# Optimization experiments

Hardware: AMD Instinct MI355X
Metric: run time of the kernel (lower is better)

Reference implementation:

```python
import math
import jax, jax.numpy as jnp
import numpy as np

DIM = 4096
N_HEADS = 32
N_KV_HEADS = 8
HEAD_DIM = DIM // N_HEADS        # 128
N_REP = N_HEADS // N_KV_HEADS    # 4
BSZ = 1
SEQ = 2048
ROPE_THETA = 500000.0


def setup_inputs() -> dict:
    key = jax.random.key(0)
    ks = jax.random.split(key, 5)
    scale = 1.0 / math.sqrt(DIM)
    x = jax.random.normal(ks[0], (BSZ, SEQ, DIM), dtype=jnp.float32)
    wq = jax.random.normal(ks[1], (N_HEADS * HEAD_DIM, DIM), dtype=jnp.float32) * scale
    wk = jax.random.normal(ks[2], (N_KV_HEADS * HEAD_DIM, DIM), dtype=jnp.float32) * scale
    wv = jax.random.normal(ks[3], (N_KV_HEADS * HEAD_DIM, DIM), dtype=jnp.float32) * scale
    wo = jax.random.normal(ks[4], (N_HEADS * HEAD_DIM, DIM), dtype=jnp.float32).T * scale
    wo = jnp.asarray(wo)  # [DIM, N_HEADS*HEAD_DIM] like nn.Linear(in=heads*hd, out=dim).weight
    # RoPE tables: freqs_cis[t, j] = exp(i * t * theta^{-2j/head_dim}), j in [0, head_dim/2)
    inv_freq = 1.0 / (ROPE_THETA ** (np.arange(0, HEAD_DIM, 2, dtype=np.float32) / HEAD_DIM))
    t = np.arange(SEQ, dtype=np.float32)
    ang = np.outer(t, inv_freq)  # [SEQ, HEAD_DIM//2]
    freqs_cos = jnp.asarray(np.cos(ang), dtype=jnp.float32)
    freqs_sin = jnp.asarray(np.sin(ang), dtype=jnp.float32)
    # additive causal mask [SEQ, SEQ]
    mask = jnp.where(jnp.tril(jnp.ones((SEQ, SEQ), dtype=bool)), 0.0, -1e9).astype(jnp.float32)
    return {"x": x, "wq": wq, "wk": wk, "wv": wv, "wo": wo,
            "freqs_cos": freqs_cos, "freqs_sin": freqs_sin, "mask": mask}


def _apply_rope(xh, cos, sin):
    # xh: [b, s, h, head_dim]; cos/sin: [s, head_dim//2]
    b, s, h, d = xh.shape
    xr = xh.reshape(b, s, h, d // 2, 2)
    x0, x1 = xr[..., 0], xr[..., 1]
    c = cos[None, :, None, :]
    sn = sin[None, :, None, :]
    o0 = x0 * c - x1 * sn
    o1 = x0 * sn + x1 * c
    return jnp.stack([o0, o1], axis=-1).reshape(b, s, h, d)


def reference(x, wq, wk, wv, wo, freqs_cos, freqs_sin, mask):
    bsz, seqlen, _ = x.shape
    xq = (x @ wq.T).reshape(bsz, seqlen, N_HEADS, HEAD_DIM)
    xk = (x @ wk.T).reshape(bsz, seqlen, N_KV_HEADS, HEAD_DIM)
    xv = (x @ wv.T).reshape(bsz, seqlen, N_KV_HEADS, HEAD_DIM)
    xq = _apply_rope(xq, freqs_cos, freqs_sin)
    xk = _apply_rope(xk, freqs_cos, freqs_sin)
    # repeat_kv (GQA expansion)
    keys = jnp.repeat(xk, N_REP, axis=2)    # [b, s, N_HEADS, hd]
    values = jnp.repeat(xv, N_REP, axis=2)
    scores = jnp.einsum('bqhd,bkhd->bhqk', xq, keys) / math.sqrt(HEAD_DIM)
    scores = scores + mask[None, None, :, :]
    scores = jax.nn.softmax(scores.astype(jnp.float32), axis=-1).astype(xq.dtype)
    out = jnp.einsum('bhqk,bkhd->bqhd', scores, values)
    out = out.reshape(bsz, seqlen, N_HEADS * HEAD_DIM)
    return out @ wo.T
```

## Files before the change

kernel.cpp:

```cpp
#include <hip/hip_runtime.h>
#include <math.h>
#include <stdint.h>
#include <stddef.h>


typedef __attribute__((ext_vector_type(8))) short bf16x8;
typedef __attribute__((ext_vector_type(4))) short bf16x4;
typedef __attribute__((ext_vector_type(4))) float f32x4;
typedef unsigned short u16;

#define NEG_BIG (-1.0e9f)
#define MFMA32(a, b, c) __builtin_amdgcn_mfma_f32_16x16x32_bf16(a, b, c, 0, 0, 0)

__device__ __forceinline__ float bf2f(u16 b) {
    return __uint_as_float(((unsigned int)b) << 16);
}
__device__ __forceinline__ u16 f2bf(float f) {
    unsigned int u = __float_as_uint(f);
    u += 0x7fff + ((u >> 16) & 1);
    return (u16)(u >> 16);
}
__device__ __forceinline__ void gld_lds16(short* lds, const u16* g) {
    __builtin_amdgcn_global_load_lds(
        (const __attribute__((address_space(1))) void*)g,
        (__attribute__((address_space(3))) void*)lds, 16, 0, 0);
}

__global__ __launch_bounds__(256) void cvt_bf16(const float* __restrict__ src,
                                                u16* __restrict__ dst, int n) {
    int i = (blockIdx.x * blockDim.x + threadIdx.x) * 8;
    if (i >= n) return;
    float4 a, b;
    __builtin_memcpy(&a, src + i, 16);
    __builtin_memcpy(&b, src + i + 4, 16);
    bf16x8 o;
    o[0] = (short)f2bf(a.x); o[1] = (short)f2bf(a.y);
    o[2] = (short)f2bf(a.z); o[3] = (short)f2bf(a.w);
    o[4] = (short)f2bf(b.x); o[5] = (short)f2bf(b.y);
    o[6] = (short)f2bf(b.z); o[7] = (short)f2bf(b.w);
    __builtin_memcpy(dst + i, &o, 16);
}

template <int OUT>
__device__ __forceinline__ void gemm_tile_bt(const u16* __restrict__ A,
                                             const u16* __restrict__ B,
                                             void* __restrict__ C,
                                             int mb, int nb, int N, int K,
                                             short* As, short* Bs) {
    const int t = threadIdx.x;
    const int lane = t & 63, wave = t >> 6;
    const int l15 = lane & 15, quad = lane >> 4;
    const int wm = (wave >> 1) * 64, wn = (wave & 1) * 64;
    f32x4 acc[4][4] = {};

    const int r0 = t >> 2, cc0 = (t & 3) * 8;
    const u16* Ap0 = A + (size_t)(mb * 128 + r0) * K + cc0;
    const u16* Ap1 = Ap0 + (size_t)64 * K;
    const u16* Bp0 = B + (size_t)(nb * 128 + r0) * K + cc0;
    const u16* Bp1 = Bp0 + (size_t)64 * K;
    short* asd0 = As + t * 8; short* asd1 = As + (t + 256) * 8;
    short* bsd0 = Bs + t * 8; short* bsd1 = Bs + (t + 256) * 8;

    int aoff[4], boff[4];
#pragma unroll
    for (int i = 0; i < 4; ++i) {
        aoff[i] = (wm + i * 16 + l15) * 32 + quad * 8;
        boff[i] = (wn + i * 16 + l15) * 32 + quad * 8;
    }

    for (int kb = 0; kb < K; kb += 32) {
        gld_lds16(asd0, Ap0 + kb);
        gld_lds16(asd1, Ap1 + kb);
        gld_lds16(bsd0, Bp0 + kb);
        gld_lds16(bsd1, Bp1 + kb);
        __syncthreads();
        bf16x8 af[4], bfr[4];
#pragma unroll
        for (int i = 0; i < 4; ++i) __builtin_memcpy(&af[i], As + aoff[i], 16);
#pragma unroll
        for (int j = 0; j < 4; ++j) __builtin_memcpy(&bfr[j], Bs + boff[j], 16);
#pragma unroll
        for (int i = 0; i < 4; ++i)
#pragma unroll
            for (int j = 0; j < 4; ++j)
                acc[i][j] = MFMA32(af[i], bfr[j], acc[i][j]);
        __syncthreads();
    }

#pragma unroll
    for (int i = 0; i < 4; ++i)
#pragma unroll
        for (int j = 0; j < 4; ++j) {
            if (OUT == 2) {
                int col = nb * 128 + wn + j * 16 + l15;
                int row0 = mb * 128 + wm + i * 16 + quad * 4;
                bf16x4 v;
#pragma unroll
                for (int r = 0; r < 4; ++r) v[r] = (short)f2bf(acc[i][j][r]);
                __builtin_memcpy((u16*)C + (size_t)col * 2048 + row0, &v, 8);
            } else {
#pragma unroll
                for (int r = 0; r < 4; ++r) {
                    int row = mb * 128 + wm + i * 16 + quad * 4 + r;
                    int col = nb * 128 + wn + j * 16 + l15;
                    if (OUT == 1)
                        ((float*)C)[(size_t)row * N + col] = acc[i][j][r];
                    else
                        ((u16*)C)[(size_t)row * N + col] = f2bf(acc[i][j][r]);
                }
            }
        }
}

__global__ __launch_bounds__(256) void qkv_proj(
    const u16* __restrict__ x,
    const u16* __restrict__ wq, const u16* __restrict__ wk,
    const u16* __restrict__ wv,
    u16* __restrict__ Q, u16* __restrict__ Kc, u16* __restrict__ Vt) {
    __shared__ __align__(16) short As[128 * 32];
    __shared__ __align__(16) short Bs[128 * 32];
    int mb = blockIdx.x, y = blockIdx.y;
    if (y < 32)
        gemm_tile_bt<0>(x, wq, Q, mb, y, 4096, 4096, As, Bs);
    else if (y < 40)
        gemm_tile_bt<0>(x, wk, Kc, mb, y - 32, 1024, 4096, As, Bs);
    else
        gemm_tile_bt<2>(x, wv, Vt, mb, y - 40, 1024, 4096, As, Bs);
}

__global__ __launch_bounds__(256) void oproj(
    const u16* __restrict__ A, const u16* __restrict__ wo,
    float* __restrict__ out) {
    __shared__ __align__(16) short As[128 * 32];
    __shared__ __align__(16) short Bs[128 * 32];
    gemm_tile_bt<1>(A, wo, out, blockIdx.x, blockIdx.y, 4096, 4096, As, Bs);
}

__global__ void rope_kernel(u16* __restrict__ X,
                            const float* __restrict__ cosb,
                            const float* __restrict__ sinb, int nheads) {
    int idx = blockIdx.x * blockDim.x + threadIdx.x;
    int total = 2048 * nheads * 64;
    if (idx >= total) return;
    int i = idx % 64;
    int h = (idx / 64) % nheads;
    int s = idx / (64 * nheads);
    u16* p = X + (size_t)s * nheads * 128 + h * 128 + 2 * i;
    float x0 = bf2f(p[0]), x1 = bf2f(p[1]);
    float c = cosb[s * 64 + i], sn = sinb[s * 64 + i];
    p[0] = f2bf(x0 * c - x1 * sn);
    p[1] = f2bf(x0 * sn + x1 * c);
}

__device__ __forceinline__ int kswz(int row, int cs) {
    int f = (row & 3) | ((row & 8) >> 1);
    return row * 128 + ((cs ^ f) << 3);
}

template <bool MASKED>
__device__ __forceinline__ void fa_step_lds(
    const short* __restrict__ Kl, const short* __restrict__ Vl,
    int kb, int q0, int l15, int quad,
    const int (&koff)[8], const int (&voff)[8],
    const bf16x8 (&qf)[4], f32x4 (&o)[8], float& m, float& l) {
    const float scale = 0.08838834764831845f;

    bf16x8 kf[8];
#pragma unroll
    for (int i = 0; i < 8; ++i) __builtin_memcpy(&kf[i], Kl + koff[i], 16);
    f32x4 s0 = {0, 0, 0, 0}, s1 = {0, 0, 0, 0};
#pragma unroll
    for (int c = 0; c < 4; ++c) {
        s0 = MFMA32(kf[c], qf[c], s0);
        s1 = MFMA32(kf[4 + c], qf[c], s1);
    }

    bf16x8 vf[8];
#pragma unroll
    for (int n = 0; n < 8; ++n) __builtin_memcpy(&vf[n], Vl + voff[n], 16);

    float sv0[4], sv1[4];
    const int q = q0 + l15;
#pragma unroll
    for (int r = 0; r < 4; ++r) {
        sv0[r] = s0[r] * scale;
        sv1[r] = s1[r] * scale;
        if (MASKED) {
            if (kb + 8 * quad + r > q) sv0[r] = NEG_BIG;
            if (kb + 8 * quad + 4 + r > q) sv1[r] = NEG_BIG;
        }
    }

    float mx = fmaxf(fmaxf(fmaxf(sv0[0], sv0[1]), fmaxf(sv0[2], sv0[3])),
                     fmaxf(fmaxf(sv1[0], sv1[1]), fmaxf(sv1[2], sv1[3])));
    mx = fmaxf(mx, __shfl_xor(mx, 16));
    mx = fmaxf(mx, __shfl_xor(mx, 32));

    float alpha = 1.0f;
    if (!__all(mx <= m + 8.0f)) {
        float mnew = fmaxf(m, mx);
        alpha = __expf(m - mnew);
        float aO[4];
#pragma unroll
        for (int r = 0; r < 4; ++r) aO[r] = __shfl(alpha, quad * 20 + r);
#pragma unroll
        for (int n = 0; n < 8; ++n)
#pragma unroll
            for (int r = 0; r < 4; ++r) o[n][r] *= aO[r];
        m = mnew;
    }

    float p0[4], p1[4], sum = 0.f;
#pragma unroll
    for (int r = 0; r < 4; ++r) {
        p0[r] = __expf(sv0[r] - m);
        p1[r] = __expf(sv1[r] - m);
        sum += p0[r] + p1[r];
    }
    sum += __shfl_xor(sum, 16);
    sum += __shfl_xor(sum, 32);
    l = l * alpha + sum;

    bf16x8 pa;
#pragma unroll
    for (int r = 0; r < 4; ++r) {
        pa[r] = (short)f2bf(p0[r]);
        pa[4 + r] = (short)f2bf(p1[r]);
    }

#pragma unroll
    for (int n = 0; n < 8; ++n) o[n] = MFMA32(pa, vf[n], o[n]);
}

__device__ __forceinline__ void fa_task(
    const u16* __restrict__ Q, const u16* __restrict__ Kc,
    const u16* __restrict__ Vt, u16* __restrict__ O,
    short* __restrict__ Kl0, short* __restrict__ Vl0,
    int q0, int nbt, int h, int kvh, int t) {
    const int lane = t & 63;
    const int l15 = lane & 15, quad = lane >> 4;

    bf16x8 qf[4];
    const u16* qp = Q + (size_t)(q0 + l15) * 4096 + h * 128 + quad * 8;
#pragma unroll
    for (int c = 0; c < 4; ++c) __builtin_memcpy(&qf[c], qp + c * 32, 16);

    const u16* ksrc[2]; short* kdst[2];
    const u16* vsrc[2]; short* vdst[2];
#pragma unroll
    for (int r = 0; r < 2; ++r) {
        int row = (t >> 4) + 16 * r;
        int slot = t & 15;
        int f = (row & 3) | ((row & 8) >> 1);
        int cs = slot ^ f;
        ksrc[r] = Kc + (size_t)row * 1024 + kvh * 128 + cs * 8;
        kdst[r] = Kl0 + (t + 256 * r) * 8;
        int rowv = (t >> 2) + 64 * r;
        int sv = t & 3;
        vsrc[r] = Vt + (size_t)(kvh * 128 + rowv) * 2048 + sv * 8;
        vdst[r] = Vl0 + (t + 256 * r) * 8;
    }

    const int rk0 = 8 * (l15 >> 2) + (l15 & 3);
    int koff[8], voff[8];
#pragma unroll
    for (int c = 0; c < 4; ++c) {
        koff[c] = kswz(rk0, quad + c * 4);
        koff[4 + c] = kswz(rk0 + 4, quad + c * 4);
    }
#pragma unroll
    for (int n = 0; n < 8; ++n) voff[n] = (n * 16 + l15) * 32 + quad * 8;

    f32x4 o[8] = {};
    float m = NEG_BIG, l = 0.f;
    const int my_nb = (q0 + 47) / 32;

    {
        gld_lds16(kdst[0], ksrc[0]);
        gld_lds16(kdst[1], ksrc[1]);
        gld_lds16(vdst[0], vsrc[0]);
        gld_lds16(vdst[1], vsrc[1]);
    }
    __syncthreads();

    for (int ib = 0; ib < nbt; ++ib) {
        if (ib + 1 < nbt) {
            int kb = (ib + 1) * 32;
            int bo = ((ib + 1) & 1) * 4096;
            gld_lds16(kdst[0] + bo, ksrc[0] + (size_t)kb * 1024);
            gld_lds16(kdst[1] + bo, ksrc[1] + (size_t)kb * 1024);
            gld_lds16(vdst[0] + bo, vsrc[0] + kb);
            gld_lds16(vdst[1] + bo, vsrc[1] + kb);
        }
        if (ib < my_nb) {
            const short* Kl = Kl0 + (ib & 1) * 4096;
            const short* Vl = Vl0 + (ib & 1) * 4096;
            if (ib == my_nb - 1)
                fa_step_lds<true>(Kl, Vl, ib * 32, q0, l15, quad, koff, voff,
                                  qf, o, m, l);
            else
                fa_step_lds<false>(Kl, Vl, ib * 32, q0, l15, quad, koff, voff,
                                   qf, o, m, l);
        }
        __syncthreads();
    }

    float inv[4];
#pragma unroll
    for (int r = 0; r < 4; ++r) inv[r] = 1.f / __shfl(l, quad * 20 + r);
#pragma unroll
    for (int n = 0; n < 8; ++n)
#pragma unroll
        for (int r = 0; r < 4; ++r) {
            int row = q0 + quad * 4 + r;
            O[(size_t)row * 4096 + h * 128 + n * 16 + l15] =
                f2bf(o[n][r] * inv[r]);
        }
}

__global__ __launch_bounds__(256) void flash_attn(
    const u16* __restrict__ Q, const u16* __restrict__ Kc,
    const u16* __restrict__ Vt, u16* __restrict__ O) {
    __shared__ __align__(16) short Kl[2 * 32 * 128];
    __shared__ __align__(16) short Vl[2 * 128 * 32];
    const int pp = blockIdx.x;
    const int h = blockIdx.y;
    const int kvh = h >> 2;
    const int t = threadIdx.x, wave = t >> 6;
    fa_task(Q, Kc, Vt, O, Kl, Vl, pp * 64 + wave * 16, 2 * pp + 2, h, kvh, t);
    const int tb = 31 - pp;
    fa_task(Q, Kc, Vt, O, Kl, Vl, tb * 64 + (3 - wave) * 16, 2 * tb + 2, h,
            kvh, t);
}

extern "C" void kernel_launch(void* const* d_in, const int* in_sizes, int n_in,
                              void* d_out, int out_size, void* d_ws,
                              size_t ws_size, hipStream_t stream) {
    const float* x  = (const float*)d_in[0];
    const float* wq = (const float*)d_in[1];
    const float* wk = (const float*)d_in[2];
    const float* wv = (const float*)d_in[3];
    const float* wo = (const float*)d_in[4];
    const float* fc = (const float*)d_in[5];
    const float* fs = (const float*)d_in[6];
    float* out = (float*)d_out;

    const int NX = 2048 * 4096;
    const int NQW = 4096 * 4096;
    const int NKW = 1024 * 4096;
    const int NKV = 2048 * 1024;

    u16* Q   = (u16*)d_ws;
    u16* Kc  = Q   + NX;
    u16* Vt  = Kc  + NKV;
    u16* Ao  = Vt  + NKV;
    u16* xb  = Ao  + NX;
    u16* wqb = xb  + NX;
    u16* wkb = wqb + NQW;
    u16* wvb = wkb + NKW;
    u16* wob = wvb + NKW;

    cvt_bf16<<<NX / (256 * 8), 256, 0, stream>>>(x, xb, NX);
    cvt_bf16<<<NQW / (256 * 8), 256, 0, stream>>>(wq, wqb, NQW);
    cvt_bf16<<<NKW / (256 * 8), 256, 0, stream>>>(wk, wkb, NKW);
    cvt_bf16<<<NKW / (256 * 8), 256, 0, stream>>>(wv, wvb, NKW);
    cvt_bf16<<<NQW / (256 * 8), 256, 0, stream>>>(wo, wob, NQW);

    qkv_proj<<<dim3(16, 48), 256, 0, stream>>>(xb, wqb, wkb, wvb, Q, Kc, Vt);
    rope_kernel<<<(2048 * 32 * 64 + 255) / 256, 256, 0, stream>>>(Q, fc, fs, 32);
    rope_kernel<<<(2048 * 8 * 64 + 255) / 256, 256, 0, stream>>>(Kc, fc, fs, 8);
    flash_attn<<<dim3(16, 32), 256, 0, stream>>>(Q, Kc, Vt, Ao);
    oproj<<<dim3(16, 32), 256, 0, stream>>>(Ao, wob, out);
}
```

Baseline: 533.9 us.

## Replace GEMM tiles with 8-wave 256-wide double-buffered pipelined kernels

Measured after the change: 512.5 us. 1.04x faster.

```diff
diff --git a/kernel.cpp b/kernel.cpp
--- a/kernel.cpp
+++ b/kernel.cpp
@@ -41,99 +41,167 @@
     __builtin_memcpy(dst + i, &o, 16);
 }
 
-template <int OUT>
-__device__ __forceinline__ void gemm_tile_bt(const u16* __restrict__ A,
-                                             const u16* __restrict__ B,
-                                             void* __restrict__ C,
-                                             int mb, int nb, int N, int K,
-                                             short* As, short* Bs) {
+
+#define G8_STGA(bf_, ks_, kt_)                                               \
+    {                                                                        \
+        _Pragma("unroll") for (int r_ = 0; r_ < RA; ++r_)                    \
+            gld_lds16(Ad + (bf_) * AT + (ks_) * AH + r_ * 4096,              \
+                      Ag + gK * r_ + (size_t)(kt_) * 64 + (ks_) * 32);       \
+    }
+#define G8_STGB(bf_, ks_, kt_)                                               \
+    {                                                                        \
+        _Pragma("unroll") for (int r_ = 0; r_ < RB; ++r_)                    \
+            gld_lds16(Bd + (bf_) * BT + (ks_) * BH + r_ * 4096,              \
+                      Bg + gK * r_ + (size_t)(kt_) * 64 + (ks_) * 32);       \
+    }
+#define G8_PHASE(bf_, ks_, mh_, RDB_, STAGE_, WAIT_)                         \
+    {                                                                        \
+        if (RDB_) {                                                          \
+            _Pragma("unroll") for (int n_ = 0; n_ < 4; ++n_)                 \
+                __builtin_memcpy(&bfr[n_], Bs + (bf_) * BT + (ks_) * BH +    \
+                                               bbase + n_ * 512, 16);        \
+        }                                                                    \
+        _Pragma("unroll") for (int i_ = 0; i_ < 4; ++i_)                     \
+            __builtin_memcpy(&af[i_], S + (bf_) * AT + (ks_) * AH + abase +  \
+                                          ((mh_) * 64 + i_ * 16) * 32, 16);  \
+        STAGE_;                                                              \
+        __builtin_amdgcn_s_barrier();                                        \
+        __builtin_amdgcn_s_setprio(1);                                       \
+        _Pragma("unroll") for (int i_ = 0; i_ < 4; ++i_)                     \
+            _Pragma("unroll") for (int n_ = 0; n_ < 4; ++n_)                 \
+                acc[(mh_) * 4 + i_][n_] =                                    \
+                    MFMA32(af[i_], bfr[n_], acc[(mh_) * 4 + i_][n_]);        \
+        __builtin_amdgcn_s_setprio(0);                                       \
+        asm volatile("s_waitcnt lgkmcnt(0)" ::: "memory");                   \
+        WAIT_;                                                               \
+        __builtin_amdgcn_s_barrier();                                        \
+    }
+
+template <int BM, int BN, int MH, int OUT>
+__device__ __forceinline__ void gemm8p(const u16* __restrict__ A,
+                                       const u16* __restrict__ B,
+                                       void* __restrict__ C,
+                                       int mb, int nb, int N, int K,
+                                       short* __restrict__ S) {
+    constexpr int AT = BM * 64, BT = BN * 64;
+    constexpr int AH = BM * 32, BH = BN * 32;
+    constexpr int RA = BM / 128, RB = BN / 128;
+    short* const Bs = S + 2 * AT;
+
     const int t = threadIdx.x;
-    const int lane = t & 63, wave = t >> 6;
-    const int l15 = lane & 15, quad = lane >> 4;
-    const int wm = (wave >> 1) * 64, wn = (wave & 1) * 64;
-    f32x4 acc[4][4] = {};
-
-    const int r0 = t >> 2, cc0 = (t & 3) * 8;
-    const u16* Ap0 = A + (size_t)(mb * 128 + r0) * K + cc0;
-    const u16* Ap1 = Ap0 + (size_t)64 * K;
-    const u16* Bp0 = B + (size_t)(nb * 128 + r0) * K + cc0;
-    const u16* Bp1 = Bp0 + (size_t)64 * K;
-    short* asd0 = As + t * 8; short* asd1 = As + (t + 256) * 8;
-    short* bsd0 = Bs + t * 8; short* bsd1 = Bs + (t + 256) * 8;
-
-    int aoff[4], boff[4];
-#pragma unroll
-    for (int i = 0; i < 4; ++i) {
-        aoff[i] = (wm + i * 16 + l15) * 32 + quad * 8;
-        boff[i] = (wn + i * 16 + l15) * 32 + quad * 8;
-    }
-
-    for (int kb = 0; kb < K; kb += 32) {
-        gld_lds16(asd0, Ap0 + kb);
-        gld_lds16(asd1, Ap1 + kb);
-        gld_lds16(bsd0, Bp0 + kb);
-        gld_lds16(bsd1, Bp1 + kb);
-        __syncthreads();
-        bf16x8 af[4], bfr[4];
-#pragma unroll
-        for (int i = 0; i < 4; ++i) __builtin_memcpy(&af[i], As + aoff[i], 16);
-#pragma unroll
-        for (int j = 0; j < 4; ++j) __builtin_memcpy(&bfr[j], Bs + boff[j], 16);
-#pragma unroll
-        for (int i = 0; i < 4; ++i)
-#pragma unroll
-            for (int j = 0; j < 4; ++j)
-                acc[i][j] = MFMA32(af[i], bfr[j], acc[i][j]);
-        __syncthreads();
-    }
-
-#pragma unroll
-    for (int i = 0; i < 4; ++i)
+    const int lane = t & 63, l15 = lane & 15, quad = lane >> 4;
+    const int wid = t >> 6, wr = wid >> 2, wc = wid & 3;
+
+    const int srow = t >> 2, sslot = t & 3;
+    const u16* const Ag = A + (size_t)(mb * BM + srow) * K + sslot * 8;
+    const u16* const Bg = B + (size_t)(nb * BN + srow) * K + sslot * 8;
+    short* const Ad = S + t * 8;
+    short* const Bd = Bs + t * 8;
+    const size_t gK = (size_t)128 * K;
+
+    const int abase = (wr * (BM / 2) + l15) * 32 + quad * 8;
+    const int bbase = (wc * 64 + l15) * 32 + quad * 8;
+
+    f32x4 acc[MH * 4][4] = {};
+    bf16x8 af[4], bfr[4];
+
+    G8_STGA(0, 0, 0); G8_STGB(0, 0, 0);
+    G8_STGA(0, 1, 0); G8_STGB(0, 1, 0);
+    G8_STGA(1, 0, 1); G8_STGB(1, 0, 1);
+    if constexpr (MH == 2) {
+        asm volatile("s_waitcnt vmcnt(4)" ::: "memory");
+    } else {
+        asm volatile("s_waitcnt vmcnt(6)" ::: "memory");
+    }
+    __builtin_amdgcn_s_barrier();
+
+    const int nIt = K >> 7;
+    if constexpr (MH == 2) {
+        for (int it = 0; it < nIt; ++it) {
+            const int k0 = 2 * it, k1 = k0 + 1;
+            const bool nl = (it < nIt - 1);
+            G8_PHASE(0, 0, 0, true,  G8_STGA(1, 1, k1), );
+            G8_PHASE(0, 0, 1, false, G8_STGB(1, 1, k1), );
+            G8_PHASE(0, 1, 0, true,  if (nl) G8_STGA(0, 0, k0 + 2), );
+            G8_PHASE(0, 1, 1, false, if (nl) G8_STGB(0, 0, k0 + 2),
+                     if (nl) { asm volatile("s_waitcnt vmcnt(4)" ::: "memory"); }
+                     else    { asm volatile("s_waitcnt vmcnt(0)" ::: "memory"); });
+            G8_PHASE(1, 0, 0, true,  if (nl) G8_STGA(0, 1, k0 + 2), );
+            G8_PHASE(1, 0, 1, false, if (nl) G8_STGB(0, 1, k0 + 2), );
+            G8_PHASE(1, 1, 0, true,  if (nl) G8_STGA(1, 0, k1 + 2), );
+            G8_PHASE(1, 1, 1, false, if (nl) G8_STGB(1, 0, k1 + 2),
+                     if (nl) { asm volatile("s_waitcnt vmcnt(4)" ::: "memory"); });
+        }
+    } else {
+        for (int it = 0; it < nIt - 1; ++it) {
+            const int k0 = 2 * it, k1 = k0 + 1;
+            G8_PHASE(0, 0, 0, true, { G8_STGA(1, 1, k1); G8_STGB(1, 1, k1); },
+                     asm volatile("s_waitcnt vmcnt(6)" ::: "memory"));
+            G8_PHASE(0, 1, 0, true, { G8_STGA(0, 0, k0 + 2); G8_STGB(0, 0, k0 + 2); },
+                     asm volatile("s_waitcnt vmcnt(6)" ::: "memory"));
+            G8_PHASE(1, 0, 0, true, { G8_STGA(0, 1, k0 + 2); G8_STGB(0, 1, k0 + 2); },
+                     asm volatile("s_waitcnt vmcnt(6)" ::: "memory"));
+            G8_PHASE(1, 1, 0, true, { G8_STGA(1, 0, k1 + 2); G8_STGB(1, 0, k1 + 2); },
+                     asm volatile("s_waitcnt vmcnt(6)" ::: "memory"));
+        }
+        {
+            const int k1 = (K >> 6) - 1;
+            G8_PHASE(0, 0, 0, true, { G8_STGA(1, 1, k1); G8_STGB(1, 1, k1); },
+                     asm volatile("s_waitcnt vmcnt(6)" ::: "memory"));
+            G8_PHASE(0, 1, 0, true, ,
+                     asm volatile("s_waitcnt vmcnt(3)" ::: "memory"));
+            G8_PHASE(1, 0, 0, true, ,
+                     asm volatile("s_waitcnt vmcnt(0)" ::: "memory"));
+            G8_PHASE(1, 1, 0, true, , );
+        }
+    }
+
+#pragma unroll
+    for (int i8 = 0; i8 < MH * 4; ++i8) {
+        const int rowb = mb * BM + wr * (BM / 2) + (i8 >> 2) * 64 +
+                         (i8 & 3) * 16 + quad * 4;
 #pragma unroll
         for (int j = 0; j < 4; ++j) {
+            const int col = nb * BN + wc * 64 + j * 16 + l15;
             if (OUT == 2) {
-                int col = nb * 128 + wn + j * 16 + l15;
-                int row0 = mb * 128 + wm + i * 16 + quad * 4;
                 bf16x4 v;
 #pragma unroll
-                for (int r = 0; r < 4; ++r) v[r] = (short)f2bf(acc[i][j][r]);
-                __builtin_memcpy((u16*)C + (size_t)col * 2048 + row0, &v, 8);
+                for (int r = 0; r < 4; ++r) v[r] = (short)f2bf(acc[i8][j][r]);
+                __builtin_memcpy((u16*)C + (size_t)col * 2048 + rowb, &v, 8);
+            } else if (OUT == 1) {
+#pragma unroll
+                for (int r = 0; r < 4; ++r)
+                    ((float*)C)[(size_t)(rowb + r) * N + col] = acc[i8][j][r];
             } else {
 #pragma unroll
-                for (int r = 0; r < 4; ++r) {
-                    int row = mb * 128 + wm + i * 16 + quad * 4 + r;
-                    int col = nb * 128 + wn + j * 16 + l15;
-                    if (OUT == 1)
-                        ((float*)C)[(size_t)row * N + col] = acc[i][j][r];
-                    else
-                        ((u16*)C)[(size_t)row * N + col] = f2bf(acc[i][j][r]);
-                }
+                for (int r = 0; r < 4; ++r)
+                    ((u16*)C)[(size_t)(rowb + r) * N + col] =
+                        f2bf(acc[i8][j][r]);
             }
         }
-}
-
-__global__ __launch_bounds__(256) void qkv_proj(
+    }
+}
+
+__global__ __launch_bounds__(512, 2) void qkv_proj8(
     const u16* __restrict__ x,
     const u16* __restrict__ wq, const u16* __restrict__ wk,
     const u16* __restrict__ wv,
     u16* __restrict__ Q, u16* __restrict__ Kc, u16* __restrict__ Vt) {
-    __shared__ __align__(16) short As[128 * 32];
-    __shared__ __align__(16) short Bs[128 * 32];
-    int mb = blockIdx.x, y = blockIdx.y;
-    if (y < 32)
-        gemm_tile_bt<0>(x, wq, Q, mb, y, 4096, 4096, As, Bs);
-    else if (y < 40)
-        gemm_tile_bt<0>(x, wk, Kc, mb, y - 32, 1024, 4096, As, Bs);
+    __shared__ __align__(16) short S[65536];
+    const int mb = blockIdx.x, y = blockIdx.y;
+    if (y < 16)
+        gemm8p<256, 256, 2, 0>(x, wq, Q, mb, y, 4096, 4096, S);
+    else if (y < 20)
+        gemm8p<256, 256, 2, 0>(x, wk, Kc, mb, y - 16, 1024, 4096, S);
     else
-        gemm_tile_bt<2>(x, wv, Vt, mb, y - 40, 1024, 4096, As, Bs);
-}
-
-__global__ __launch_bounds__(256) void oproj(
+        gemm8p<256, 256, 2, 2>(x, wv, Vt, mb, y - 20, 1024, 4096, S);
+}
+
+__global__ __launch_bounds__(512, 2) void oproj8(
     const u16* __restrict__ A, const u16* __restrict__ wo,
     float* __restrict__ out) {
-    __shared__ __align__(16) short As[128 * 32];
-    __shared__ __align__(16) short Bs[128 * 32];
-    gemm_tile_bt<1>(A, wo, out, blockIdx.x, blockIdx.y, 4096, 4096, As, Bs);
+    __shared__ __align__(16) short S[49152];
+    gemm8p<128, 256, 1, 1>(A, wo, out, blockIdx.x, blockIdx.y, 4096, 4096, S);
 }
 
 __global__ void rope_kernel(u16* __restrict__ X,
@@ -366,9 +434,9 @@
     cvt_bf16<<<NKW / (256 * 8), 256, 0, stream>>>(wv, wvb, NKW);
     cvt_bf16<<<NQW / (256 * 8), 256, 0, stream>>>(wo, wob, NQW);
 
-    qkv_proj<<<dim3(16, 48), 256, 0, stream>>>(xb, wqb, wkb, wvb, Q, Kc, Vt);
+    qkv_proj8<<<dim3(8, 24), 512, 0, stream>>>(xb, wqb, wkb, wvb, Q, Kc, Vt);
     rope_kernel<<<(2048 * 32 * 64 + 255) / 256, 256, 0, stream>>>(Q, fc, fs, 32);
     rope_kernel<<<(2048 * 8 * 64 + 255) / 256, 256, 0, stream>>>(Kc, fc, fs, 8);
     flash_attn<<<dim3(16, 32), 256, 0, stream>>>(Q, Kc, Vt, Ao);
-    oproj<<<dim3(16, 32), 256, 0, stream>>>(Ao, wob, out);
-}
+    oproj8<<<dim3(16, 16), 512, 0, stream>>>(Ao, wob, out);
+}
```
